# Kernel tuning notes

Measured on AMD Instinct MI355X. Metric: run time of the kernel, lower is better.

Reference implementation:

```python
import jax, jax.numpy as jnp
import numpy as np

LATENT = 3
HIDDEN = 16
INP = LATENT + 1  # prev_z cat action
B = 1048576


def setup_inputs() -> dict:
    key = jax.random.key(0)
    ks = jax.random.split(key, 11)
    s_ih = 1.0 / np.sqrt(HIDDEN)
    return {
        "prev_z": jax.random.normal(ks[0], (B, LATENT), jnp.float32),
        "action": jax.random.normal(ks[1], (B, 1), jnp.float32),
        "prev_h": jax.random.normal(ks[2], (B, HIDDEN), jnp.float32),
        # GRUCell params (torch layout: [3*H, in] and [3*H, H], gate order r,z,n)
        "W_ih": jax.random.uniform(ks[3], (3 * HIDDEN, INP), jnp.float32, -s_ih, s_ih),
        "W_hh": jax.random.uniform(ks[4], (3 * HIDDEN, HIDDEN), jnp.float32, -s_ih, s_ih),
        "b_ih": jax.random.uniform(ks[5], (3 * HIDDEN,), jnp.float32, -s_ih, s_ih),
        "b_hh": jax.random.uniform(ks[6], (3 * HIDDEN,), jnp.float32, -s_ih, s_ih),
        # prior heads
        "W_mu": jax.random.uniform(ks[7], (LATENT, HIDDEN), jnp.float32, -s_ih, s_ih),
        "b_mu": jax.random.uniform(ks[8], (LATENT,), jnp.float32, -s_ih, s_ih),
        "W_lv": jax.random.uniform(ks[9], (LATENT, HIDDEN), jnp.float32, -s_ih, s_ih),
        "b_lv": jax.random.uniform(ks[10], (LATENT,), jnp.float32, -s_ih, s_ih),
    }


def reference(prev_z, action, prev_h, W_ih, W_hh, b_ih, b_hh, W_mu, b_mu, W_lv, b_lv):
    x = jnp.concatenate([prev_z, action], axis=-1)              # [B, 4]
    gi = x @ W_ih.T + b_ih                                       # [B, 3H]
    gh = prev_h @ W_hh.T + b_hh                                  # [B, 3H]
    i_r, i_z, i_n = jnp.split(gi, 3, axis=-1)
    h_r, h_z, h_n = jnp.split(gh, 3, axis=-1)
    r = jax.nn.sigmoid(i_r + h_r)
    z = jax.nn.sigmoid(i_z + h_z)
    n = jnp.tanh(i_n + r * h_n)
    h = (1.0 - z) * n + z * prev_h                               # [B, H]
    mu = h @ W_mu.T + b_mu                                       # [B, 3]
    logvar = jnp.clip(h @ W_lv.T + b_lv, -5.0, 5.0)              # [B, 3]
    return mu, logvar, h
```

## Files before the change

kernel.cpp:

```cpp
#include <hip/hip_runtime.h>

#define TPB 64
#define LOG2E 1.44269504088896340736f

typedef _Float16 half8 __attribute__((ext_vector_type(8)));
typedef _Float16 half4 __attribute__((ext_vector_type(4)));
typedef __fp16  fp16x2 __attribute__((ext_vector_type(2)));
typedef float f32x4 __attribute__((ext_vector_type(4)));

__device__ __forceinline__ half8 pack8(float4 lo, float4 hi) {
    union { fp16x2 p[4]; half8 h; } u;
    u.p[0] = __builtin_amdgcn_cvt_pkrtz(lo.x, lo.y);
    u.p[1] = __builtin_amdgcn_cvt_pkrtz(lo.z, lo.w);
    u.p[2] = __builtin_amdgcn_cvt_pkrtz(hi.x, hi.y);
    u.p[3] = __builtin_amdgcn_cvt_pkrtz(hi.z, hi.w);
    return u.h;
}
__device__ __forceinline__ half4 cvt4(float4 v) {
    union { fp16x2 p[2]; half4 h; } u;
    u.p[0] = __builtin_amdgcn_cvt_pkrtz(v.x, v.y);
    u.p[1] = __builtin_amdgcn_cvt_pkrtz(v.z, v.w);
    return u.h;
}
__device__ __forceinline__ half8 cat8(half4 a, half4 b) {
    union { half4 q[2]; half8 o; } u;
    u.q[0] = a; u.q[1] = b;
    return u.o;
}
__device__ __forceinline__ void nt_store4(float* p, float4 v) {
    union { float4 s; f32x4 e; } u;
    u.s = v;
    __builtin_nontemporal_store(u.e, (f32x4*)p);
}


__global__ __launch_bounds__(64) void prep_kernel(
    const float* __restrict__ W_ih, const float* __restrict__ W_hh,
    const float* __restrict__ b_ih, const float* __restrict__ b_hh,
    const float* __restrict__ W_mu, const float* __restrict__ b_mu,
    const float* __restrict__ W_lv, const float* __restrict__ b_lv,
    void* __restrict__ wsv)
{
    _Float16* wsB = (_Float16*)wsv;
    const int l = threadIdx.x;
    const int col = l & 15, kg = l >> 4;

    #pragma unroll
    for (int t = 0; t < 4; ++t) {
        const int gate = (t == 0) ? col : (t == 1) ? (16 + col) : (32 + col);
        const float scale = (t <= 1) ? -LOG2E : -2.0f * LOG2E;
        #pragma unroll
        for (int i = 0; i < 8; ++i) {
            const int k = kg * 8 + i;
            float v = 0.f;
            if (t <= 1) {
                if (k < 16)            v = W_hh[gate * 16 + k];
                else if (k < 20)       v = W_ih[gate * 4 + (k - 16)];
            } else if (t == 2) {
                if (k >= 16 && k < 20) v = W_ih[gate * 4 + (k - 16)];
            } else {
                if (k < 16)            v = W_hh[gate * 16 + k];
            }
            wsB[t * 512 + l * 8 + i] = (_Float16)(v * scale);
        }
    }
    #pragma unroll
    for (int i = 0; i < 8; ++i) {
        const int k = kg * 8 + i;
        wsB[4 * 512 + l * 8 + i] = (_Float16)((k == col) ? 1.f : 0.f);
    }
    #pragma unroll
    for (int i = 0; i < 8; ++i) {
        const int k = kg * 8 + i;
        const int m = col;
        float v = 0.f;
        if (m < 3) {
            if (k < 16)       v = W_mu[m * 16 + k];
            else if (k == 20) v = b_mu[m];
        } else if (m < 6) {
            if (k < 16)       v = W_lv[(m - 3) * 16 + k];
            else if (k == 20) v = b_lv[m - 3];
        }
        wsB[5 * 512 + l * 8 + i] = (_Float16)v;
    }
    if (l < 16) {
        float4* b4 = (float4*)((char*)wsv + 6144);
        b4[l] = make_float4(-LOG2E * (b_ih[l] + b_hh[l]),
                            -LOG2E * (b_ih[16 + l] + b_hh[16 + l]),
                            -2.0f * LOG2E * b_ih[32 + l],
                            -2.0f * LOG2E * b_hh[32 + l]);
    }
}

template<bool EXACT>
__global__ __launch_bounds__(TPB, 4) void rssm_kernel(
    const float* __restrict__ prev_z,
    const float* __restrict__ action,
    const float* __restrict__ prev_h,
    const void*  __restrict__ wsv,
    float* __restrict__ out_mu,
    float* __restrict__ out_lv,
    float* __restrict__ out_h,
    int B)
{
    __shared__ __align__(16) float Hb[2][64 * 16];
    __shared__ __align__(8)  _Float16 XAb[64 * 4];
    __shared__ float MU[192], LV[192];

    const int lane = threadIdx.x;
    const int col = lane & 15, kg = lane >> 4;
    const int bbase = blockIdx.x * 128;
    if (!EXACT && bbase >= B) return;

    const half8* Bp = (const half8*)wsv;
    const half8 bR  = Bp[lane];
    const half8 bZ  = Bp[64 + lane];
    const half8 bNi = Bp[128 + lane];
    const half8 bNh = Bp[192 + lane];
    const half8 bHp = Bp[256 + lane];
    const half8 a2  = Bp[320 + lane];
    const float4 bias = ((const float4*)((const char*)wsv + 6144))[col];

    if constexpr (EXACT) {
        const float4* hg = (const float4*)(prev_h + (size_t)bbase * 16);
        #pragma unroll
        for (int c = 0; c < 2; ++c)
            #pragma unroll
            for (int i = 0; i < 4; ++i)
                __builtin_amdgcn_global_load_lds(
                    (const void*)(hg + c * 256 + i * 64 + lane),
                    (void*)&Hb[c][i * 256], 16, 0, 0);
        asm volatile("s_waitcnt vmcnt(4)" ::: "memory");
        __builtin_amdgcn_sched_barrier(0);
    } else {
        const float4* hg = (const float4*)prev_h;
        #pragma unroll
        for (int c = 0; c < 2; ++c)
            #pragma unroll
            for (int i = 0; i < 4; ++i) {
                const int gi = min(bbase * 4 + c * 256 + i * 64 + lane, B * 4 - 1);
                *(float4*)&Hb[c][i * 256 + lane * 4] = hg[gi];
            }
    }

    half4 zz; zz[0] = zz[1] = zz[2] = zz[3] = (_Float16)0.f;

    #pragma unroll
    for (int c = 0; c < 2; ++c) {
        const int cbase = bbase + c * 64;
        if (EXACT || cbase < B) {
            if (EXACT && c == 1) {
                asm volatile("s_waitcnt vmcnt(0)" ::: "memory");
                __builtin_amdgcn_sched_barrier(0);
            }
            float* Hc = Hb[c];

            {
                const int zr = EXACT ? (cbase + lane) : min(cbase + lane, B - 1);
                *(half4*)&XAb[lane * 4] =
                    cvt4(make_float4(prev_z[zr * 3 + 0], prev_z[zr * 3 + 1],
                                     prev_z[zr * 3 + 2], action[zr]));
            }

            #pragma unroll
            for (int t = 0; t < 4; ++t) {
                half8 a;
                if (kg < 2) {
                    const float4 p0 = *(const float4*)&Hc[(t * 16 + col) * 16 + kg * 8];
                    const float4 p1 = *(const float4*)&Hc[(t * 16 + col) * 16 + kg * 8 + 4];
                    a = pack8(p0, p1);
                } else if (kg == 2) {
                    a = cat8(*(const half4*)&XAb[(t * 16 + col) * 4], zz);
                } else {
                    a = cat8(zz, zz);
                }

                f32x4 accR  = {bias.x, bias.x, bias.x, bias.x};
                f32x4 accZ  = {bias.y, bias.y, bias.y, bias.y};
                f32x4 accNi = {bias.z, bias.z, bias.z, bias.z};
                f32x4 accNh = {bias.w, bias.w, bias.w, bias.w};
                f32x4 accHp = {0.f, 0.f, 0.f, 0.f};
                accR  = __builtin_amdgcn_mfma_f32_16x16x32_f16(a, bR,  accR,  0, 0, 0);
                accZ  = __builtin_amdgcn_mfma_f32_16x16x32_f16(a, bZ,  accZ,  0, 0, 0);
                accNi = __builtin_amdgcn_mfma_f32_16x16x32_f16(a, bNi, accNi, 0, 0, 0);
                accNh = __builtin_amdgcn_mfma_f32_16x16x32_f16(a, bNh, accNh, 0, 0, 0);
                accHp = __builtin_amdgcn_mfma_f32_16x16x32_f16(a, bHp, accHp, 0, 0, 0);

                #pragma unroll
                for (int q = 0; q < 4; ++q) {
                    const float r  = __builtin_amdgcn_rcpf(1.0f + __builtin_amdgcn_exp2f(accR[q]));
                    const float z  = __builtin_amdgcn_rcpf(1.0f + __builtin_amdgcn_exp2f(accZ[q]));
                    const float ta = fmaf(r, accNh[q], accNi[q]);
                    const float n  = fmaf(2.0f,
                                          __builtin_amdgcn_rcpf(1.0f + __builtin_amdgcn_exp2f(ta)),
                                          -1.0f);
                    const float hv = fmaf(z, accHp[q] - n, n);
                    Hc[(t * 16 + kg * 4 + q) * 16 + col] = hv;
                }

                half8 b2;
                if (kg < 2) {
                    const float4 h0 = *(const float4*)&Hc[(t * 16 + col) * 16 + kg * 8];
                    const float4 h1 = *(const float4*)&Hc[(t * 16 + col) * 16 + kg * 8 + 4];
                    b2 = pack8(h0, h1);
                } else {
                    b2 = cat8(zz, zz);
                    if (kg == 2) b2[4] = (_Float16)1.0f;
                }
                f32x4 acc2 = {0.f, 0.f, 0.f, 0.f};
                acc2 = __builtin_amdgcn_mfma_f32_16x16x32_f16(a2, b2, acc2, 0, 0, 0);

                const int mr = (t * 16 + col) * 3;
                if (kg == 0) {
                    MU[mr + 0] = acc2[0];
                    MU[mr + 1] = acc2[1];
                    MU[mr + 2] = acc2[2];
                    LV[mr + 0] = fminf(fmaxf(acc2[3], -5.0f), 5.0f);
                } else if (kg == 1) {
                    LV[mr + 1] = fminf(fmaxf(acc2[0], -5.0f), 5.0f);
                    LV[mr + 2] = fminf(fmaxf(acc2[1], -5.0f), 5.0f);
                }

                {
                    const int r = lane >> 2, w = lane & 3;
                    const float4 hv4 = *(const float4*)&Hc[(t * 16 + r) * 16 + w * 4];
                    const int orow = cbase + t * 16 + r;
                    if (EXACT || orow < B)
                        nt_store4(&out_h[(size_t)orow * 16 + w * 4], hv4);
                }
            }

            if (lane < 48) {
                const int gi = cbase * 3 + lane * 4;
                if (EXACT || gi + 3 < B * 3) {
                    nt_store4(&out_mu[gi], *(const float4*)&MU[lane * 4]);
                    nt_store4(&out_lv[gi], *(const float4*)&LV[lane * 4]);
                }
            }
        }
    }
}

extern "C" void kernel_launch(void* const* d_in, const int* in_sizes, int n_in,
                              void* d_out, int out_size, void* d_ws, size_t ws_size,
                              hipStream_t stream) {
    const float* prev_z = (const float*)d_in[0];
    const float* action = (const float*)d_in[1];
    const float* prev_h = (const float*)d_in[2];
    const float* W_ih   = (const float*)d_in[3];
    const float* W_hh   = (const float*)d_in[4];
    const float* b_ih   = (const float*)d_in[5];
    const float* b_hh   = (const float*)d_in[6];
    const float* W_mu   = (const float*)d_in[7];
    const float* b_mu   = (const float*)d_in[8];
    const float* W_lv   = (const float*)d_in[9];
    const float* b_lv   = (const float*)d_in[10];

    const int B = in_sizes[0] / 3;
    float* out    = (float*)d_out;
    float* out_mu = out;
    float* out_lv = out + (size_t)3 * B;
    float* out_h  = out + (size_t)6 * B;

    prep_kernel<<<1, 64, 0, stream>>>(W_ih, W_hh, b_ih, b_hh,
                                      W_mu, b_mu, W_lv, b_lv, d_ws);

    const int rows_per_block = 128;
    const int blocks = (B + rows_per_block - 1) / rows_per_block;
    if ((B % rows_per_block) == 0)
        rssm_kernel<true><<<blocks, TPB, 0, stream>>>(prev_z, action, prev_h, d_ws,
                                                      out_mu, out_lv, out_h, B);
    else
        rssm_kernel<false><<<blocks, TPB, 0, stream>>>(prev_z, action, prev_h, d_ws,
                                                       out_mu, out_lv, out_h, B);
}
```

Measured before the change: 41.51 us.

## Process eight row chunks per block with double-buffered prev_h prefetch

Each block now covers 512 rows in eight 64-row chunks instead of two. It prefetches prev_h into a double-buffered LDS tile via global_load_lds two chunks ahead, and stages all prev_z/action rows into LDS upfront. The aim is to amortize per-block weight loads and launch overhead and to overlap memory with MFMA compute. The risk is fewer blocks, hence lower occupancy and less latency hiding across the GPU.

```diff
diff --git a/kernel.cpp b/kernel.cpp
--- a/kernel.cpp
+++ b/kernel.cpp
@@ -1,6 +1,9 @@
 #include <hip/hip_runtime.h>
 
 #define TPB 64
+#define KCH 8
+#define CHR 64
+#define BLKR (KCH * CHR)
 #define LOG2E 1.44269504088896340736f
 
 typedef _Float16 half8 __attribute__((ext_vector_type(8)));
@@ -104,13 +107,13 @@
     int B)
 {
     __shared__ __align__(16) float Hb[2][64 * 16];
-    __shared__ __align__(8)  _Float16 XAb[64 * 4];
+    __shared__ __align__(16) float XA[BLKR * 4];
     __shared__ float MU[192], LV[192];
 
     const int lane = threadIdx.x;
     const int col = lane & 15, kg = lane >> 4;
-    const int bbase = blockIdx.x * 128;
-    if (!EXACT && bbase >= B) return;
+    const size_t bbase = (size_t)blockIdx.x * BLKR;
+    if (!EXACT && bbase >= (size_t)B) return;
 
     const half8* Bp = (const half8*)wsv;
     const half8 bR  = Bp[lane];
@@ -121,122 +124,142 @@
     const half8 a2  = Bp[320 + lane];
     const float4 bias = ((const float4*)((const char*)wsv + 6144))[col];
 
+    half4 zz; zz[0] = zz[1] = zz[2] = zz[3] = (_Float16)0.f;
+
+    auto compute_chunk = [&](int cb, int cloc, size_t cbase) {
+        float* Hc = Hb[cb];
+        #pragma unroll
+        for (int t = 0; t < 4; ++t) {
+            half8 a;
+            if (kg < 2) {
+                const float4 p0 = *(const float4*)&Hc[(t * 16 + col) * 16 + kg * 8];
+                const float4 p1 = *(const float4*)&Hc[(t * 16 + col) * 16 + kg * 8 + 4];
+                a = pack8(p0, p1);
+            } else if (kg == 2) {
+                const float4 x4 = *(const float4*)&XA[(cloc + t * 16 + col) * 4];
+                a = cat8(cvt4(x4), zz);
+            } else {
+                a = cat8(zz, zz);
+            }
+
+            f32x4 accR  = {bias.x, bias.x, bias.x, bias.x};
+            f32x4 accZ  = {bias.y, bias.y, bias.y, bias.y};
+            f32x4 accNi = {bias.z, bias.z, bias.z, bias.z};
+            f32x4 accNh = {bias.w, bias.w, bias.w, bias.w};
+            f32x4 accHp = {0.f, 0.f, 0.f, 0.f};
+            accR  = __builtin_amdgcn_mfma_f32_16x16x32_f16(a, bR,  accR,  0, 0, 0);
+            accZ  = __builtin_amdgcn_mfma_f32_16x16x32_f16(a, bZ,  accZ,  0, 0, 0);
+            accNi = __builtin_amdgcn_mfma_f32_16x16x32_f16(a, bNi, accNi, 0, 0, 0);
+            accNh = __builtin_amdgcn_mfma_f32_16x16x32_f16(a, bNh, accNh, 0, 0, 0);
+            accHp = __builtin_amdgcn_mfma_f32_16x16x32_f16(a, bHp, accHp, 0, 0, 0);
+
+            #pragma unroll
+            for (int q = 0; q < 4; ++q) {
+                const float r  = __builtin_amdgcn_rcpf(1.0f + __builtin_amdgcn_exp2f(accR[q]));
+                const float z  = __builtin_amdgcn_rcpf(1.0f + __builtin_amdgcn_exp2f(accZ[q]));
+                const float ta = fmaf(r, accNh[q], accNi[q]);
+                const float n  = fmaf(2.0f,
+                                      __builtin_amdgcn_rcpf(1.0f + __builtin_amdgcn_exp2f(ta)),
+                                      -1.0f);
+                const float hv = fmaf(z, accHp[q] - n, n);
+                Hc[(t * 16 + kg * 4 + q) * 16 + col] = hv;
+            }
+
+            half8 b2;
+            if (kg < 2) {
+                const float4 h0 = *(const float4*)&Hc[(t * 16 + col) * 16 + kg * 8];
+                const float4 h1 = *(const float4*)&Hc[(t * 16 + col) * 16 + kg * 8 + 4];
+                b2 = pack8(h0, h1);
+            } else {
+                b2 = cat8(zz, zz);
+                if (kg == 2) b2[4] = (_Float16)1.0f;
+            }
+            f32x4 acc2 = {0.f, 0.f, 0.f, 0.f};
+            acc2 = __builtin_amdgcn_mfma_f32_16x16x32_f16(a2, b2, acc2, 0, 0, 0);
+
+            const int mr = (t * 16 + col) * 3;
+            if (kg == 0) {
+                MU[mr + 0] = acc2[0];
+                MU[mr + 1] = acc2[1];
+                MU[mr + 2] = acc2[2];
+                LV[mr + 0] = fminf(fmaxf(acc2[3], -5.0f), 5.0f);
+            } else if (kg == 1) {
+                LV[mr + 1] = fminf(fmaxf(acc2[0], -5.0f), 5.0f);
+                LV[mr + 2] = fminf(fmaxf(acc2[1], -5.0f), 5.0f);
+            }
+
+            {
+                const int r = lane >> 2, w = lane & 3;
+                const float4 hv4 = *(const float4*)&Hc[(t * 16 + r) * 16 + w * 4];
+                const size_t orow = cbase + t * 16 + r;
+                if (EXACT || orow < (size_t)B)
+                    nt_store4(&out_h[orow * 16 + w * 4], hv4);
+            }
+        }
+
+        if (lane < 48) {
+            const size_t gi = cbase * 3 + lane * 4;
+            if (EXACT || gi + 3 < (size_t)B * 3) {
+                nt_store4(&out_mu[gi], *(const float4*)&MU[lane * 4]);
+                nt_store4(&out_lv[gi], *(const float4*)&LV[lane * 4]);
+            }
+        }
+    };
+
     if constexpr (EXACT) {
-        const float4* hg = (const float4*)(prev_h + (size_t)bbase * 16);
         #pragma unroll
-        for (int c = 0; c < 2; ++c)
+        for (int i = 0; i < 8; ++i) {
+            const int rl = i * 64 + lane;
+            const size_t gr = bbase + rl;
+            *(float4*)&XA[rl * 4] =
+                make_float4(prev_z[gr * 3 + 0], prev_z[gr * 3 + 1],
+                            prev_z[gr * 3 + 2], action[gr]);
+        }
+        asm volatile("s_waitcnt vmcnt(0)" ::: "memory");
+        __builtin_amdgcn_sched_barrier(0);
+
+        auto issue = [&](int c) {
+            const size_t cbase = bbase + (size_t)c * CHR;
+            const float4* hg = (const float4*)(prev_h + cbase * 16);
             #pragma unroll
             for (int i = 0; i < 4; ++i)
                 __builtin_amdgcn_global_load_lds(
-                    (const void*)(hg + c * 256 + i * 64 + lane),
-                    (void*)&Hb[c][i * 256], 16, 0, 0);
-        asm volatile("s_waitcnt vmcnt(4)" ::: "memory");
-        __builtin_amdgcn_sched_barrier(0);
+                    (const void*)(hg + i * 64 + lane),
+                    (void*)&Hb[c & 1][i * 256], 16, 0, 0);
+        };
+
+        issue(0);
+        issue(1);
+        #pragma unroll 1
+        for (int c = 0; c < KCH; ++c) {
+            if (c < KCH - 1) {
+                asm volatile("s_waitcnt vmcnt(4)" ::: "memory");
+            } else {
+                asm volatile("s_waitcnt vmcnt(0)" ::: "memory");
+            }
+            __builtin_amdgcn_sched_barrier(0);
+            compute_chunk(c & 1, c * CHR, bbase + (size_t)c * CHR);
+            if (c + 2 < KCH) {
+                __builtin_amdgcn_sched_barrier(0);
+                issue(c + 2);
+            }
+        }
     } else {
         const float4* hg = (const float4*)prev_h;
-        #pragma unroll
-        for (int c = 0; c < 2; ++c)
+        #pragma unroll 1
+        for (int c = 0; c < KCH; ++c) {
+            const size_t cbase = bbase + (size_t)c * CHR;
+            if (cbase >= (size_t)B) break;
             #pragma unroll
             for (int i = 0; i < 4; ++i) {
-                const int gi = min(bbase * 4 + c * 256 + i * 64 + lane, B * 4 - 1);
-                *(float4*)&Hb[c][i * 256 + lane * 4] = hg[gi];
-            }
-    }
-
-    half4 zz; zz[0] = zz[1] = zz[2] = zz[3] = (_Float16)0.f;
-
-    #pragma unroll
-    for (int c = 0; c < 2; ++c) {
-        const int cbase = bbase + c * 64;
-        if (EXACT || cbase < B) {
-            if (EXACT && c == 1) {
-                asm volatile("s_waitcnt vmcnt(0)" ::: "memory");
-                __builtin_amdgcn_sched_barrier(0);
-            }
-            float* Hc = Hb[c];
-
-            {
-                const int zr = EXACT ? (cbase + lane) : min(cbase + lane, B - 1);
-                *(half4*)&XAb[lane * 4] =
-                    cvt4(make_float4(prev_z[zr * 3 + 0], prev_z[zr * 3 + 1],
-                                     prev_z[zr * 3 + 2], action[zr]));
-            }
-
-            #pragma unroll
-            for (int t = 0; t < 4; ++t) {
-                half8 a;
-                if (kg < 2) {
-                    const float4 p0 = *(const float4*)&Hc[(t * 16 + col) * 16 + kg * 8];
-                    const float4 p1 = *(const float4*)&Hc[(t * 16 + col) * 16 + kg * 8 + 4];
-                    a = pack8(p0, p1);
-                } else if (kg == 2) {
-                    a = cat8(*(const half4*)&XAb[(t * 16 + col) * 4], zz);
-                } else {
-                    a = cat8(zz, zz);
-                }
-
-                f32x4 accR  = {bias.x, bias.x, bias.x, bias.x};
-                f32x4 accZ  = {bias.y, bias.y, bias.y, bias.y};
-                f32x4 accNi = {bias.z, bias.z, bias.z, bias.z};
-                f32x4 accNh = {bias.w, bias.w, bias.w, bias.w};
-                f32x4 accHp = {0.f, 0.f, 0.f, 0.f};
-                accR  = __builtin_amdgcn_mfma_f32_16x16x32_f16(a, bR,  accR,  0, 0, 0);
-                accZ  = __builtin_amdgcn_mfma_f32_16x16x32_f16(a, bZ,  accZ,  0, 0, 0);
-                accNi = __builtin_amdgcn_mfma_f32_16x16x32_f16(a, bNi, accNi, 0, 0, 0);
-                accNh = __builtin_amdgcn_mfma_f32_16x16x32_f16(a, bNh, accNh, 0, 0, 0);
-                accHp = __builtin_amdgcn_mfma_f32_16x16x32_f16(a, bHp, accHp, 0, 0, 0);
-
-                #pragma unroll
-                for (int q = 0; q < 4; ++q) {
-                    const float r  = __builtin_amdgcn_rcpf(1.0f + __builtin_amdgcn_exp2f(accR[q]));
-                    const float z  = __builtin_amdgcn_rcpf(1.0f + __builtin_amdgcn_exp2f(accZ[q]));
-                    const float ta = fmaf(r, accNh[q], accNi[q]);
-                    const float n  = fmaf(2.0f,
-                                          __builtin_amdgcn_rcpf(1.0f + __builtin_amdgcn_exp2f(ta)),
-                                          -1.0f);
-                    const float hv = fmaf(z, accHp[q] - n, n);
-                    Hc[(t * 16 + kg * 4 + q) * 16 + col] = hv;
-                }
-
-                half8 b2;
-                if (kg < 2) {
-                    const float4 h0 = *(const float4*)&Hc[(t * 16 + col) * 16 + kg * 8];
-                    const float4 h1 = *(const float4*)&Hc[(t * 16 + col) * 16 + kg * 8 + 4];
-                    b2 = pack8(h0, h1);
-                } else {
-                    b2 = cat8(zz, zz);
-                    if (kg == 2) b2[4] = (_Float16)1.0f;
-                }
-                f32x4 acc2 = {0.f, 0.f, 0.f, 0.f};
-                acc2 = __builtin_amdgcn_mfma_f32_16x16x32_f16(a2, b2, acc2, 0, 0, 0);
-
-                const int mr = (t * 16 + col) * 3;
-                if (kg == 0) {
-                    MU[mr + 0] = acc2[0];
-                    MU[mr + 1] = acc2[1];
-                    MU[mr + 2] = acc2[2];
-                    LV[mr + 0] = fminf(fmaxf(acc2[3], -5.0f), 5.0f);
-                } else if (kg == 1) {
-                    LV[mr + 1] = fminf(fmaxf(acc2[0], -5.0f), 5.0f);
-                    LV[mr + 2] = fminf(fmaxf(acc2[1], -5.0f), 5.0f);
-                }
-
-                {
-                    const int r = lane >> 2, w = lane & 3;
-                    const float4 hv4 = *(const float4*)&Hc[(t * 16 + r) * 16 + w * 4];
-                    const int orow = cbase + t * 16 + r;
-                    if (EXACT || orow < B)
-                        nt_store4(&out_h[(size_t)orow * 16 + w * 4], hv4);
-                }
-            }
-
-            if (lane < 48) {
-                const int gi = cbase * 3 + lane * 4;
-                if (EXACT || gi + 3 < B * 3) {
-                    nt_store4(&out_mu[gi], *(const float4*)&MU[lane * 4]);
-                    nt_store4(&out_lv[gi], *(const float4*)&LV[lane * 4]);
-                }
-            }
+                const size_t gi = min(cbase * 4 + i * 64 + lane, (size_t)B * 4 - 1);
+                *(float4*)&Hb[c & 1][i * 256 + lane * 4] = hg[gi];
+            }
+            const size_t zr = min(cbase + lane, (size_t)B - 1);
+            *(float4*)&XA[(c * CHR + lane) * 4] =
+                make_float4(prev_z[zr * 3 + 0], prev_z[zr * 3 + 1],
+                            prev_z[zr * 3 + 2], action[zr]);
+            compute_chunk(c & 1, c * CHR, cbase);
         }
     }
 }
@@ -265,9 +288,8 @@
     prep_kernel<<<1, 64, 0, stream>>>(W_ih, W_hh, b_ih, b_hh,
                                       W_mu, b_mu, W_lv, b_lv, d_ws);
 
-    const int rows_per_block = 128;
-    const int blocks = (B + rows_per_block - 1) / rows_per_block;
-    if ((B % rows_per_block) == 0)
+    const int blocks = (B + BLKR - 1) / BLKR;
+    if ((B % BLKR) == 0)
         rssm_kernel<true><<<blocks, TPB, 0, stream>>>(prev_z, action, prev_h, d_ws,
                                                       out_mu, out_lv, out_h, B);
     else
```

Result: slower. 43.45 us (+4.7%).
